# Optimization experiments

Measured on AMD Instinct MI355X. Metric: run time of the kernel, lower is better.

Reference implementation:

```python
import jax, jax.numpy as jnp
import numpy as np

N, C, H, W = 512, 512, 7, 7
K = 64
ALPHA = 100.0
HW = H * W


def _up13(x):
    # bilinear upsample (..., 7, 7) -> (..., 13, 13), align_corners=True
    src = jnp.arange(13, dtype=jnp.float32) * (6.0 / 12.0)
    i0 = jnp.floor(src).astype(jnp.int32)
    i1 = jnp.minimum(i0 + 1, 6)
    w = src - i0.astype(jnp.float32)
    xr = x[..., i0, :] * (1.0 - w)[:, None] + x[..., i1, :] * w[:, None]  # rows
    xc = xr[..., :, i0] * (1.0 - w) + xr[..., :, i1] * w                  # cols
    return xc


def _conv2d(x, w, b, p):
    y = jax.lax.conv_general_dilated(
        x, w, window_strides=(1, 1), padding=[(p, p), (p, p)],
        dimension_numbers=('NCHW', 'OIHW', 'NCHW'))
    return y + b[None, :, None, None]


def setup_inputs() -> dict:
    key = jax.random.key(0)
    ks = jax.random.split(key, 16)
    x = jax.random.normal(ks[0], (N, C, H, W), jnp.float32)
    centroids = jax.random.uniform(ks[1], (K, C), jnp.float32)
    # conv params initialized from centroids as in _init_params (separate params after init)
    conv_w = 2.0 * ALPHA * centroids                    # (K, C) 1x1 conv kernel
    conv_b = -ALPHA * jnp.linalg.norm(centroids, axis=1)
    ln_w = jnp.ones((7, 7), jnp.float32)
    ln_b = jnp.zeros((7, 7), jnp.float32)
    c3_w = 0.02 * jax.random.normal(ks[2], (32, 512, 3, 3), jnp.float32)
    c3_b = jnp.zeros((32,), jnp.float32)
    c5_w = 0.02 * jax.random.normal(ks[3], (32, 512, 5, 5), jnp.float32)
    c5_b = jnp.zeros((32,), jnp.float32)
    c7_w = 0.02 * jax.random.normal(ks[4], (20, 512, 7, 7), jnp.float32)
    c7_b = jnp.zeros((20,), jnp.float32)
    dw_w = 0.1 * jax.random.normal(ks[5], (7, 13), jnp.float32)
    dw_b = jnp.zeros((7,), jnp.float32)
    dh_w = 0.1 * jax.random.normal(ks[6], (7, 13), jnp.float32)
    dh_b = jnp.zeros((7,), jnp.float32)
    acc_w = 0.1 * jax.random.normal(ks[7], (1, 84), jnp.float32)  # 1x1 conv (O, I)
    acc_b = jnp.zeros((1,), jnp.float32)
    return dict(x=x, centroids=centroids, conv_w=conv_w, conv_b=conv_b,
                ln_w=ln_w, ln_b=ln_b, c3_w=c3_w, c3_b=c3_b, c5_w=c5_w, c5_b=c5_b,
                c7_w=c7_w, c7_b=c7_b, dw_w=dw_w, dw_b=dw_b, dh_w=dh_w, dh_b=dh_b,
                acc_w=acc_w, acc_b=acc_b)


def reference(x, centroids, conv_w, conv_b, ln_w, ln_b,
              c3_w, c3_b, c5_w, c5_b, c7_w, c7_b,
              dw_w, dw_b, dh_w, dh_b, acc_w, acc_b):
    # ---- CRN on the raw (un-normalized) input ----
    mu = jnp.mean(x, axis=(-2, -1), keepdims=True)
    var = jnp.mean((x - mu) ** 2, axis=(-2, -1), keepdims=True)
    h = (x - mu) / jnp.sqrt(var + 1e-5) * ln_w + ln_b          # LayerNorm([7,7])
    h = _up13(h)                                               # (N,512,13,13)
    h = jnp.concatenate([_conv2d(h, c3_w, c3_b, 1),
                         _conv2d(h, c5_w, c5_b, 2),
                         _conv2d(h, c7_w, c7_b, 3)], axis=1)   # (N,84,13,13)
    h = jnp.einsum('nchw,ow->ncho', h, dw_w) + dw_b            # width 13->7
    h = h.transpose(0, 1, 3, 2)
    h = jnp.einsum('nchw,ow->ncho', h, dh_w) + dh_b            # height 13->7
    cw = jnp.einsum('nchw,oc->nohw', h, acc_w) + acc_b[None, :, None, None]
    cw = cw.reshape(N, 1, HW)                                  # context weights

    # ---- descriptor-wise L2 normalization over channels ----
    nrm = jnp.sqrt(jnp.sum(x * x, axis=1, keepdims=True))
    xn = x / jnp.maximum(nrm, 1e-12)

    # ---- soft assignment (1x1 conv + softmax over clusters) ----
    logits = (jnp.einsum('nchw,kc->nkhw', xn, conv_w)
              + conv_b[None, :, None, None]).reshape(N, K, HW)
    sa = jax.nn.softmax(logits, axis=1)
    mask = sa * cw                                             # (N,K,HW)

    # ---- fused VLAD aggregation (same math as masked residual sum) ----
    xf = xn.reshape(N, C, HW)
    vlad = jnp.einsum('nkl,ncl->nkc', mask, xf) \
        - centroids[None, :, :] * jnp.sum(mask, axis=-1)[:, :, None]
    vlad = vlad / jnp.maximum(jnp.linalg.norm(vlad, axis=2, keepdims=True), 1e-12)
    vlad = vlad.reshape(N, K * C)
    vlad = vlad / jnp.maximum(jnp.linalg.norm(vlad, axis=1, keepdims=True), 1e-12)
    return vlad
```

## Files before the change

kernel.cpp:

```cpp
#include <hip/hip_runtime.h>
#include <math.h>

#define NI 512
#define CC 512
#define KCL 64
#define HW49 49
#define CQ 25088
#define AP 260
#define GP 68
#define XQP 132

__device__ __forceinline__ float Uval(int i, int u) {
    if (i & 1) return (u == ((i - 1) >> 1) || u == ((i + 1) >> 1)) ? 0.5f : 0.0f;
    return (u == (i >> 1)) ? 1.0f : 0.0f;
}

__global__ __launch_bounds__(256) void kG(
    const float* __restrict__ c3w, const float* __restrict__ c5w, const float* __restrict__ c7w,
    const float* __restrict__ dww, const float* __restrict__ dhw, const float* __restrict__ accw,
    const float* __restrict__ lnw, const float* __restrict__ lnb,
    float* __restrict__ Gmat, float* __restrict__ Gl)
{
    const int c = blockIdx.x;
    const int t = threadIdx.x;
    __shared__ float dh[91], dw[91];
    __shared__ float Fh3[147], Fw3[147], Fh5[245], Fw5[245], Fh7[343], Fw7[343];
    __shared__ float wa3[9], wa5[25], wa7[49];
    __shared__ float Gtmp[2401];
    if (t < 91) dh[t] = dhw[t];
    if (t >= 128 && t < 219) dw[t - 128] = dww[t - 128];
    __syncthreads();
    for (int idx = t; idx < 147; idx += 256) {
        int oh = idx / 21, r = idx % 21, u = r / 3, dy = r % 3;
        float sh = 0.f, sw = 0.f;
        for (int i = 0; i < 13; i++) { int y = i - dy + 1; if (y >= 0 && y < 13) { float uu = Uval(i, u); sh += dh[oh * 13 + y] * uu; sw += dw[oh * 13 + y] * uu; } }
        Fh3[idx] = sh; Fw3[idx] = sw;
    }
    for (int idx = t; idx < 245; idx += 256) {
        int oh = idx / 35, r = idx % 35, u = r / 5, dy = r % 5;
        float sh = 0.f, sw = 0.f;
        for (int i = 0; i < 13; i++) { int y = i - dy + 2; if (y >= 0 && y < 13) { float uu = Uval(i, u); sh += dh[oh * 13 + y] * uu; sw += dw[oh * 13 + y] * uu; } }
        Fh5[idx] = sh; Fw5[idx] = sw;
    }
    for (int idx = t; idx < 343; idx += 256) {
        int oh = idx / 49, r = idx % 49, u = r / 7, dy = r % 7;
        float sh = 0.f, sw = 0.f;
        for (int i = 0; i < 13; i++) { int y = i - dy + 3; if (y >= 0 && y < 13) { float uu = Uval(i, u); sh += dh[oh * 13 + y] * uu; sw += dw[oh * 13 + y] * uu; } }
        Fh7[idx] = sh; Fw7[idx] = sw;
    }
    if (t < 9)               { float s = 0.f; for (int co = 0; co < 32; co++) s += accw[co]      * c3w[(size_t)(co * 512 + c) * 9  + t];        wa3[t] = s; }
    if (t >= 32 && t < 57)   { int q = t - 32; float s = 0.f; for (int co = 0; co < 32; co++) s += accw[32 + co] * c5w[(size_t)(co * 512 + c) * 25 + q]; wa5[q] = s; }
    if (t >= 64 && t < 113)  { int q = t - 64; float s = 0.f; for (int co = 0; co < 20; co++) s += accw[64 + co] * c7w[(size_t)(co * 512 + c) * 49 + q]; wa7[q] = s; }
    __syncthreads();
    for (int o = t; o < 2401; o += 256) {
        int q = o / 49, p = o % 49;
        int u = q / 7, v = q % 7, ow = p / 7, oh = p % 7;
        float acc = 0.f;
        #pragma unroll
        for (int dy = 0; dy < 3; dy++) { float fh = Fh3[(oh * 7 + u) * 3 + dy];
            #pragma unroll
            for (int dx = 0; dx < 3; dx++) acc += wa3[dy * 3 + dx] * fh * Fw3[(ow * 7 + v) * 3 + dx]; }
        #pragma unroll
        for (int dy = 0; dy < 5; dy++) { float fh = Fh5[(oh * 7 + u) * 5 + dy];
            #pragma unroll
            for (int dx = 0; dx < 5; dx++) acc += wa5[dy * 5 + dx] * fh * Fw5[(ow * 7 + v) * 5 + dx]; }
        #pragma unroll
        for (int dy = 0; dy < 7; dy++) { float fh = Fh7[(oh * 7 + u) * 7 + dy];
            #pragma unroll
            for (int dx = 0; dx < 7; dx++) acc += wa7[dy * 7 + dx] * fh * Fw7[(ow * 7 + v) * 7 + dx]; }
        Gtmp[o] = acc;
        Gmat[(size_t)c * 2401 + o] = acc * lnw[q];
    }
    __syncthreads();
    if (t < 49) {
        float s = 0.f;
        for (int q = 0; q < 49; q++) s += Gtmp[q * 49 + t] * lnb[q];
        Gl[c * 49 + t] = s;
    }
}

__global__ void kCb(const float* __restrict__ c3b, const float* __restrict__ c5b, const float* __restrict__ c7b,
                    const float* __restrict__ dww, const float* __restrict__ dwb,
                    const float* __restrict__ dhw, const float* __restrict__ dhb,
                    const float* __restrict__ accw, const float* __restrict__ accb,
                    const float* __restrict__ Gl, float* __restrict__ Cb)
{
    __shared__ float A0s, A1s, Sdw[7], Sdh[7];
    int t = threadIdx.x;
    if (t == 0) {
        float a0 = 0.f, a1 = 0.f;
        for (int co = 0; co < 84; co++) {
            float aw = accw[co]; a0 += aw;
            float b = (co < 32) ? c3b[co] : ((co < 64) ? c5b[co - 32] : c7b[co - 64]);
            a1 += aw * b;
        }
        A0s = a0; A1s = a1;
    }
    if (t < 7)             { float s = 0.f; for (int xx = 0; xx < 13; xx++) s += dww[t * 13 + xx]; Sdw[t] = s; }
    if (t >= 8 && t < 15)  { int oh = t - 8; float s = 0.f; for (int y = 0; y < 13; y++) s += dhw[oh * 13 + y]; Sdh[oh] = s; }
    __syncthreads();
    if (t < 49) {
        int ow = t / 7, oh = t % 7;
        float g = 0.f;
        for (int c = 0; c < 512; c++) g += Gl[c * 49 + t];
        Cb[t] = A1s * Sdw[ow] * Sdh[oh] + A0s * (dwb[ow] * Sdh[oh] + dhb[oh]) + accb[0] + g;
    }
}

__global__ __launch_bounds__(256) void kCw1(const float* __restrict__ x,
    const float* __restrict__ Gmat, float* __restrict__ part)
{
    __shared__ float As[49 * AP];
    __shared__ float Gs[49 * GP];
    const int b = blockIdx.x;
    const int nt = b >> 8, ks = b & 255;
    const int n0 = nt * 256;
    const int t = threadIdx.x;
    const int tn = t >> 3;
    const int tp = t & 7;
    float acc[8][8];
    #pragma unroll
    for (int j = 0; j < 8; j++)
        #pragma unroll
        for (int m = 0; m < 8; m++) acc[j][m] = 0.f;
    for (int kk = 0; kk < 2; kk++) {
        const int c = ks * 2 + kk;
        for (int i = t; i < 12544; i += 256) {
            int nr = i / 49, q = i - nr * 49;
            As[q * AP + nr] = x[(size_t)(n0 + nr) * CQ + (size_t)c * 49 + q];
        }
        for (int i = t; i < 2401; i += 256) {
            int q = i / 49, p = i - q * 49;
            Gs[q * GP + p] = Gmat[(size_t)c * 2401 + i];
        }
        for (int i = t; i < 735; i += 256) {
            int q = i / 15, pc = 49 + (i - q * 15);
            Gs[q * GP + pc] = 0.f;
        }
        __syncthreads();
        {
            float s = 0.f, ss = 0.f;
            for (int q = 0; q < 49; q++) { float v = As[q * AP + t]; s += v; ss += v * v; }
            float mu = s * (1.f / 49.f);
            float var = ss * (1.f / 49.f) - mu * mu;
            float rs = 1.f / sqrtf(var + 1e-5f);
            for (int q = 0; q < 49; q++) As[q * AP + t] = (As[q * AP + t] - mu) * rs;
        }
        __syncthreads();
        for (int q = 0; q < 49; q++) {
            float4 a0 = *(const float4*)&As[q * AP + tn * 8];
            float4 a1 = *(const float4*)&As[q * AP + tn * 8 + 4];
            float4 g0 = *(const float4*)&Gs[q * GP + tp * 8];
            float4 g1 = *(const float4*)&Gs[q * GP + tp * 8 + 4];
            float av[8] = {a0.x, a0.y, a0.z, a0.w, a1.x, a1.y, a1.z, a1.w};
            float gv[8] = {g0.x, g0.y, g0.z, g0.w, g1.x, g1.y, g1.z, g1.w};
            #pragma unroll
            for (int j = 0; j < 8; j++)
                #pragma unroll
                for (int m = 0; m < 8; m++) acc[j][m] += av[j] * gv[m];
        }
        __syncthreads();
    }
    #pragma unroll
    for (int j = 0; j < 8; j++) {
        #pragma unroll
        for (int m = 0; m < 8; m++) {
            int p = tp * 8 + m;
            if (p < 49) As[(tn * 8 + j) * 49 + p] = acc[j][m];
        }
    }
    __syncthreads();
    {
        float* dst = part + (size_t)ks * CQ + (size_t)n0 * 49;
        for (int i = t; i < 12544; i += 256) dst[i] = As[i];
    }
}

__global__ __launch_bounds__(512) void kLog(const float* __restrict__ x,
    const float* __restrict__ convw, const float* __restrict__ convb,
    const float* __restrict__ part, const float* __restrict__ Cbg,
    float* __restrict__ maskr, float* __restrict__ msum)
{
    __shared__ float xq[49 * XQP];
    __shared__ float lg[64 * 52];
    __shared__ float ps[8 * 56];
    __shared__ float rn[49], cwl[49], smax[49], sinv[49];
    __shared__ float cb[64];
    __shared__ float pmx[392], psm[392];
    const int n = blockIdx.x;
    const int t = threadIdx.x;
    const int lane = t & 63;
    const int kw = __builtin_amdgcn_readfirstlane(t >> 6);
    const float* xp = x + (size_t)n * CQ;

    if (t < 392) {
        int p = t >> 3, q = t & 7;
        const float* bp = part + (size_t)(q * 32) * CQ + (size_t)n * 49 + p;
        float s0 = 0.f, s1 = 0.f, s2 = 0.f, s3 = 0.f;
        for (int i = 0; i < 32; i += 4) {
            s0 += bp[(size_t)(i + 0) * CQ];
            s1 += bp[(size_t)(i + 1) * CQ];
            s2 += bp[(size_t)(i + 2) * CQ];
            s3 += bp[(size_t)(i + 3) * CQ];
        }
        psm[t] = (s0 + s1) + (s2 + s3);
    }
    if (t >= 448) cb[t - 448] = convb[t - 448];
    __syncthreads();
    if (t < 49) {
        float s = Cbg[t];
        #pragma unroll
        for (int q = 0; q < 8; q++) s += psm[t * 8 + q];
        cwl[t] = s;
    }

    float a[8] = {0.f, 0.f, 0.f, 0.f, 0.f, 0.f, 0.f, 0.f};
    float rs_part = 0.f;
    for (int qt = 0; qt < 4; qt++) {
        __syncthreads();
        for (int idx = t; idx < 1568; idx += 512) {
            int cg = idx / 49, l = idx - cg * 49;
            const float* src = xp + (size_t)(qt * 128 + cg * 4) * 49 + l;
            float4 v;
            v.x = src[0]; v.y = src[49]; v.z = src[98]; v.w = src[147];
            *(float4*)&xq[l * XQP + cg * 4] = v;
        }
        __syncthreads();
        if (lane < 49) {
            const float* row = &xq[lane * XQP + kw * 16];
            #pragma unroll
            for (int c4 = 0; c4 < 4; c4++) {
                float4 v = *(const float4*)(row + c4 * 4);
                rs_part += v.x * v.x + v.y * v.y + v.z * v.z + v.w * v.w;
            }
        }
        {
            const int lr = (lane < 49) ? lane : 48;
            const float* xrow = &xq[lr * XQP];
            const float* wb = convw + (size_t)(kw * 8) * 512 + qt * 128;
            for (int c4 = 0; c4 < 32; c4++) {
                float4 xv = *(const float4*)(xrow + c4 * 4);
                #pragma unroll
                for (int j = 0; j < 8; j++) {
                    float4 wv = *(const float4*)&wb[j * 512 + c4 * 4];
                    a[j] += wv.x * xv.x + wv.y * xv.y + wv.z * xv.z + wv.w * xv.w;
                }
            }
        }
    }
    if (lane < 49) ps[kw * 56 + lane] = rs_part;
    __syncthreads();
    if (t < 49) {
        float s = 0.f;
        #pragma unroll
        for (int q = 0; q < 8; q++) s += ps[q * 56 + t];
        rn[t] = 1.f / fmaxf(sqrtf(s), 1e-12f);
    }
    __syncthreads();
    if (lane < 49) {
        float r = rn[lane];
        #pragma unroll
        for (int j = 0; j < 8; j++) lg[(kw * 8 + j) * 52 + lane] = a[j] * r + cb[kw * 8 + j];
    }
    __syncthreads();
    if (t < 392) {
        int l = t >> 3, kq = t & 7;
        float m = -3.402823466e38f;
        #pragma unroll
        for (int j = 0; j < 8; j++) m = fmaxf(m, lg[(kq * 8 + j) * 52 + l]);
        pmx[t] = m;
    }
    __syncthreads();
    if (t < 49) {
        float m = pmx[t * 8];
        #pragma unroll
        for (int q = 1; q < 8; q++) m = fmaxf(m, pmx[t * 8 + q]);
        smax[t] = m;
    }
    __syncthreads();
    if (t < 392) {
        int l = t >> 3, kq = t & 7;
        float m = smax[l], s = 0.f;
        #pragma unroll
        for (int j = 0; j < 8; j++) s += __expf(lg[(kq * 8 + j) * 52 + l] - m);
        psm[t] = s;
    }
    __syncthreads();
    if (t < 49) {
        float s = 0.f;
        #pragma unroll
        for (int q = 0; q < 8; q++) s += psm[t * 8 + q];
        sinv[t] = 1.f / s;
    }
    __syncthreads();
    if (t < 392) {
        int l = t >> 3, kq = t & 7;
        float m = smax[l], si = sinv[l] * cwl[l];
        #pragma unroll
        for (int j = 0; j < 8; j++) {
            int idx = (kq * 8 + j) * 52 + l;
            lg[idx] = __expf(lg[idx] - m) * si;
        }
    }
    __syncthreads();
    {
        float msr[8];
        #pragma unroll
        for (int j = 0; j < 8; j++) {
            float s = 0.f;
            for (int l = 0; l < 49; l++) s += lg[(kw * 8 + j) * 52 + l];
            msr[j] = s;
        }
        if (lane == 0) {
            #pragma unroll
            for (int j = 0; j < 8; j++) msum[n * 64 + kw * 8 + j] = msr[j];
        }
    }
    for (int o = t; o < 3136; o += 512) {
        int k = o / 49, l = o - k * 49;
        maskr[(size_t)n * 3136 + o] = lg[k * 52 + l] * rn[l];
    }
}

__global__ __launch_bounds__(512) void kVd(const float* __restrict__ x,
    const float* __restrict__ maskr, const float* __restrict__ msum,
    const float* __restrict__ cent, float* __restrict__ out)
{
    __shared__ float xh[12560];
    __shared__ float lg[64 * 52];
    __shared__ float ssq[64], scl[64];
    const int n = blockIdx.x;
    const int t = threadIdx.x;
    const int lane = t & 63;
    const int kw = __builtin_amdgcn_readfirstlane(t >> 6);
    const float* xp = x + (size_t)n * CQ;
    for (int i = t; i < 3136; i += 512) { int k = i / 49, l = i - k * 49; lg[k * 52 + l] = maskr[(size_t)n * 3136 + i]; }
    for (int i = t; i < 192; i += 512) { lg[(i / 3) * 52 + 49 + (i % 3)] = 0.f; }
    float msr[8];
    #pragma unroll
    for (int j = 0; j < 8; j++) msr[j] = msum[n * 64 + kw * 8 + j];
    const int c0 = lane * 4;
    float accA[8][4], accB[8][4];
    #pragma unroll
    for (int j = 0; j < 8; j++)
        #pragma unroll
        for (int ci = 0; ci < 4; ci++) { accA[j][ci] = 0.f; accB[j][ci] = 0.f; }
    for (int i4 = t; i4 < 3136; i4 += 512)
        *(float4*)&xh[i4 * 4] = *(const float4*)&xp[12544 + i4 * 4];
    if (t < 16) xh[12544 + t] = 0.f;
    __syncthreads();
    for (int lq = 0; lq < 13; lq++) {
        float xr[4][4];
        #pragma unroll
        for (int ci = 0; ci < 4; ci++)
            #pragma unroll
            for (int dl = 0; dl < 4; dl++)
                xr[ci][dl] = xh[(c0 + ci) * 49 + lq * 4 + dl];
        #pragma unroll
        for (int j = 0; j < 8; j++) {
            float4 mv = *(const float4*)&lg[(kw * 8 + j) * 52 + lq * 4];
            #pragma unroll
            for (int ci = 0; ci < 4; ci++)
                accB[j][ci] += mv.x * xr[ci][0] + mv.y * xr[ci][1] + mv.z * xr[ci][2] + mv.w * xr[ci][3];
        }
    }
    __syncthreads();
    for (int i4 = t; i4 < 3136; i4 += 512)
        *(float4*)&xh[i4 * 4] = *(const float4*)&xp[i4 * 4];
    if (t < 16) xh[12544 + t] = 0.f;
    __syncthreads();
    for (int lq = 0; lq < 13; lq++) {
        float xr[4][4];
        #pragma unroll
        for (int ci = 0; ci < 4; ci++)
            #pragma unroll
            for (int dl = 0; dl < 4; dl++)
                xr[ci][dl] = xh[(c0 + ci) * 49 + lq * 4 + dl];
        #pragma unroll
        for (int j = 0; j < 8; j++) {
            float4 mv = *(const float4*)&lg[(kw * 8 + j) * 52 + lq * 4];
            #pragma unroll
            for (int ci = 0; ci < 4; ci++)
                accA[j][ci] += mv.x * xr[ci][0] + mv.y * xr[ci][1] + mv.z * xr[ci][2] + mv.w * xr[ci][3];
        }
    }
    float ssr[8];
    #pragma unroll
    for (int j = 0; j < 8; j++) {
        int k = kw * 8 + j;
        float ms = msr[j];
        float4 ca = *(const float4*)&cent[(size_t)k * 512 + c0];
        float4 cbv = *(const float4*)&cent[(size_t)k * 512 + 256 + c0];
        accA[j][0] -= ca.x * ms; accA[j][1] -= ca.y * ms; accA[j][2] -= ca.z * ms; accA[j][3] -= ca.w * ms;
        accB[j][0] -= cbv.x * ms; accB[j][1] -= cbv.y * ms; accB[j][2] -= cbv.z * ms; accB[j][3] -= cbv.w * ms;
        float s = 0.f;
        #pragma unroll
        for (int ci = 0; ci < 4; ci++) s += accA[j][ci] * accA[j][ci] + accB[j][ci] * accB[j][ci];
        ssr[j] = s;
    }
    #pragma unroll
    for (int j = 0; j < 8; j++)
        for (int off = 32; off >= 1; off >>= 1) ssr[j] += __shfl_xor(ssr[j], off, 64);
    if (lane == 0) {
        #pragma unroll
        for (int j = 0; j < 8; j++) ssq[kw * 8 + j] = ssr[j];
    }
    __syncthreads();
    if (t < 64) {
        float nrm = sqrtf(ssq[t]);
        float inv = 1.f / fmaxf(nrm, 1e-12f);
        float sk = nrm * inv;
        float g = sk * sk;
        #pragma unroll
        for (int off = 32; off >= 1; off >>= 1) g += __shfl_xor(g, off, 64);
        scl[t] = inv * (1.f / fmaxf(sqrtf(g), 1e-12f));
    }
    __syncthreads();
    #pragma unroll
    for (int j = 0; j < 8; j++) {
        int k = kw * 8 + j;
        float s2 = scl[k];
        float4 o1 = make_float4(accA[j][0] * s2, accA[j][1] * s2, accA[j][2] * s2, accA[j][3] * s2);
        float4 o2 = make_float4(accB[j][0] * s2, accB[j][1] * s2, accB[j][2] * s2, accB[j][3] * s2);
        *(float4*)&out[(size_t)n * 32768 + (size_t)k * 512 + c0] = o1;
        *(float4*)&out[(size_t)n * 32768 + (size_t)k * 512 + 256 + c0] = o2;
    }
}

extern "C" void kernel_launch(void* const* d_in, const int* in_sizes, int n_in,
                              void* d_out, int out_size, void* d_ws, size_t ws_size,
                              hipStream_t stream)
{
    const float* x     = (const float*)d_in[0];
    const float* cent  = (const float*)d_in[1];
    const float* convw = (const float*)d_in[2];
    const float* convb = (const float*)d_in[3];
    const float* lnw   = (const float*)d_in[4];
    const float* lnb   = (const float*)d_in[5];
    const float* c3w   = (const float*)d_in[6];
    const float* c3b   = (const float*)d_in[7];
    const float* c5w   = (const float*)d_in[8];
    const float* c5b   = (const float*)d_in[9];
    const float* c7w   = (const float*)d_in[10];
    const float* c7b   = (const float*)d_in[11];
    const float* dww   = (const float*)d_in[12];
    const float* dwb   = (const float*)d_in[13];
    const float* dhw   = (const float*)d_in[14];
    const float* dhb   = (const float*)d_in[15];
    const float* accw  = (const float*)d_in[16];
    const float* accb  = (const float*)d_in[17];
    float* out = (float*)d_out;

    char* ws = (char*)d_ws;
    float* Gmat  = (float*)(ws);
    float* Gl    = (float*)(ws + 4917248);
    float* Cb    = (float*)(ws + 5017600);
    float* part  = (float*)(ws + 5017856);
    float* maskr = (float*)(ws + 30707968);
    float* msumW = (float*)(ws + 37130496);

    kG   <<<512, 256, 0, stream>>>(c3w, c5w, c7w, dww, dhw, accw, lnw, lnb, Gmat, Gl);
    kCb  <<<1,   64,  0, stream>>>(c3b, c5b, c7b, dww, dwb, dhw, dhb, accw, accb, Gl, Cb);
    kCw1 <<<512, 256, 0, stream>>>(x, Gmat, part);
    kLog <<<512, 512, 0, stream>>>(x, convw, convb, part, Cb, maskr, msumW);
    kVd  <<<512, 512, 0, stream>>>(x, maskr, msumW, cent, out);
}
```

Measured before the change: 200.7 us.

## Double-buffer x staging in kLog and stripe channels in kVd to avoid bank conflicts

kLog now prefetches the next 128-channel slice of x into registers and writes it into a second shared-memory buffer while the current slice is being used. This overlaps global loads with the logits dot products and removes one barrier per iteration. The partial-sum reduction is respread across all waves, and the conv bias load moves to the first threads. kVd changes each lane's channels from four contiguous ones to a stride of 64, which avoids LDS bank conflicts on the 49-stride reads, at the cost of scalar rather than float4 centroid loads and output stores.

```diff
diff --git a/kernel.cpp b/kernel.cpp
--- a/kernel.cpp
+++ b/kernel.cpp
@@ -181,7 +181,7 @@
     const float* __restrict__ part, const float* __restrict__ Cbg,
     float* __restrict__ maskr, float* __restrict__ msum)
 {
-    __shared__ float xq[49 * XQP];
+    __shared__ float xq[2][49 * XQP];
     __shared__ float lg[64 * 52];
     __shared__ float ps[8 * 56];
     __shared__ float rn[49], cwl[49], smax[49], sinv[49];
@@ -193,9 +193,22 @@
     const int kw = __builtin_amdgcn_readfirstlane(t >> 6);
     const float* xp = x + (size_t)n * CQ;
 
-    if (t < 392) {
-        int p = t >> 3, q = t & 7;
-        const float* bp = part + (size_t)(q * 32) * CQ + (size_t)n * 49 + p;
+    int scg[4], sl[4];
+    #pragma unroll
+    for (int s = 0; s < 4; s++) {
+        int idx = t + s * 512;
+        scg[s] = idx / 49; sl[s] = idx - scg[s] * 49;
+    }
+    float4 r[4];
+    #pragma unroll
+    for (int s = 0; s < 4; s++) {
+        if (s < 3 || t < 32) {
+            const float* src = xp + (size_t)(scg[s] * 4) * 49 + sl[s];
+            r[s].x = src[0]; r[s].y = src[49]; r[s].z = src[98]; r[s].w = src[147];
+        }
+    }
+    if (lane < 49) {
+        const float* bp = part + (size_t)(kw * 32) * CQ + (size_t)n * 49 + lane;
         float s0 = 0.f, s1 = 0.f, s2 = 0.f, s3 = 0.f;
         for (int i = 0; i < 32; i += 4) {
             s0 += bp[(size_t)(i + 0) * CQ];
@@ -203,9 +216,23 @@
             s2 += bp[(size_t)(i + 2) * CQ];
             s3 += bp[(size_t)(i + 3) * CQ];
         }
-        psm[t] = (s0 + s1) + (s2 + s3);
-    }
-    if (t >= 448) cb[t - 448] = convb[t - 448];
+        psm[lane * 8 + kw] = (s0 + s1) + (s2 + s3);
+    }
+    if (t < 64) cb[t] = convb[t];
+
+    float a[8] = {0.f, 0.f, 0.f, 0.f, 0.f, 0.f, 0.f, 0.f};
+    float rs_part = 0.f;
+
+    #pragma unroll
+    for (int s = 0; s < 4; s++)
+        if (s < 3 || t < 32) *(float4*)&xq[0][sl[s] * XQP + scg[s] * 4] = r[s];
+    #pragma unroll
+    for (int s = 0; s < 4; s++) {
+        if (s < 3 || t < 32) {
+            const float* src = xp + (size_t)(128 + scg[s] * 4) * 49 + sl[s];
+            r[s].x = src[0]; r[s].y = src[49]; r[s].z = src[98]; r[s].w = src[147];
+        }
+    }
     __syncthreads();
     if (t < 49) {
         float s = Cbg[t];
@@ -213,21 +240,10 @@
         for (int q = 0; q < 8; q++) s += psm[t * 8 + q];
         cwl[t] = s;
     }
-
-    float a[8] = {0.f, 0.f, 0.f, 0.f, 0.f, 0.f, 0.f, 0.f};
-    float rs_part = 0.f;
     for (int qt = 0; qt < 4; qt++) {
-        __syncthreads();
-        for (int idx = t; idx < 1568; idx += 512) {
-            int cg = idx / 49, l = idx - cg * 49;
-            const float* src = xp + (size_t)(qt * 128 + cg * 4) * 49 + l;
-            float4 v;
-            v.x = src[0]; v.y = src[49]; v.z = src[98]; v.w = src[147];
-            *(float4*)&xq[l * XQP + cg * 4] = v;
-        }
-        __syncthreads();
+        const float* buf = xq[qt & 1];
         if (lane < 49) {
-            const float* row = &xq[lane * XQP + kw * 16];
+            const float* row = &buf[lane * XQP + kw * 16];
             #pragma unroll
             for (int c4 = 0; c4 < 4; c4++) {
                 float4 v = *(const float4*)(row + c4 * 4);
@@ -236,7 +252,7 @@
         }
         {
             const int lr = (lane < 49) ? lane : 48;
-            const float* xrow = &xq[lr * XQP];
+            const float* xrow = &buf[lr * XQP];
             const float* wb = convw + (size_t)(kw * 8) * 512 + qt * 128;
             for (int c4 = 0; c4 < 32; c4++) {
                 float4 xv = *(const float4*)(xrow + c4 * 4);
@@ -247,6 +263,21 @@
                 }
             }
         }
+        if (qt < 3) {
+            #pragma unroll
+            for (int s = 0; s < 4; s++)
+                if (s < 3 || t < 32) *(float4*)&xq[(qt + 1) & 1][sl[s] * XQP + scg[s] * 4] = r[s];
+            if (qt < 2) {
+                #pragma unroll
+                for (int s = 0; s < 4; s++) {
+                    if (s < 3 || t < 32) {
+                        const float* src = xp + (size_t)((qt + 2) * 128 + scg[s] * 4) * 49 + sl[s];
+                        r[s].x = src[0]; r[s].y = src[49]; r[s].z = src[98]; r[s].w = src[147];
+                    }
+                }
+            }
+            __syncthreads();
+        }
     }
     if (lane < 49) ps[kw * 56 + lane] = rs_part;
     __syncthreads();
@@ -258,9 +289,9 @@
     }
     __syncthreads();
     if (lane < 49) {
-        float r = rn[lane];
-        #pragma unroll
-        for (int j = 0; j < 8; j++) lg[(kw * 8 + j) * 52 + lane] = a[j] * r + cb[kw * 8 + j];
+        float r0 = rn[lane];
+        #pragma unroll
+        for (int j = 0; j < 8; j++) lg[(kw * 8 + j) * 52 + lane] = a[j] * r0 + cb[kw * 8 + j];
     }
     __syncthreads();
     if (t < 392) {
@@ -339,7 +370,6 @@
     float msr[8];
     #pragma unroll
     for (int j = 0; j < 8; j++) msr[j] = msum[n * 64 + kw * 8 + j];
-    const int c0 = lane * 4;
     float accA[8][4], accB[8][4];
     #pragma unroll
     for (int j = 0; j < 8; j++)
@@ -355,7 +385,7 @@
         for (int ci = 0; ci < 4; ci++)
             #pragma unroll
             for (int dl = 0; dl < 4; dl++)
-                xr[ci][dl] = xh[(c0 + ci) * 49 + lq * 4 + dl];
+                xr[ci][dl] = xh[(lane + 64 * ci) * 49 + lq * 4 + dl];
         #pragma unroll
         for (int j = 0; j < 8; j++) {
             float4 mv = *(const float4*)&lg[(kw * 8 + j) * 52 + lq * 4];
@@ -375,7 +405,7 @@
         for (int ci = 0; ci < 4; ci++)
             #pragma unroll
             for (int dl = 0; dl < 4; dl++)
-                xr[ci][dl] = xh[(c0 + ci) * 49 + lq * 4 + dl];
+                xr[ci][dl] = xh[(lane + 64 * ci) * 49 + lq * 4 + dl];
         #pragma unroll
         for (int j = 0; j < 8; j++) {
             float4 mv = *(const float4*)&lg[(kw * 8 + j) * 52 + lq * 4];
@@ -389,13 +419,15 @@
     for (int j = 0; j < 8; j++) {
         int k = kw * 8 + j;
         float ms = msr[j];
-        float4 ca = *(const float4*)&cent[(size_t)k * 512 + c0];
-        float4 cbv = *(const float4*)&cent[(size_t)k * 512 + 256 + c0];
-        accA[j][0] -= ca.x * ms; accA[j][1] -= ca.y * ms; accA[j][2] -= ca.z * ms; accA[j][3] -= ca.w * ms;
-        accB[j][0] -= cbv.x * ms; accB[j][1] -= cbv.y * ms; accB[j][2] -= cbv.z * ms; accB[j][3] -= cbv.w * ms;
         float s = 0.f;
         #pragma unroll
-        for (int ci = 0; ci < 4; ci++) s += accA[j][ci] * accA[j][ci] + accB[j][ci] * accB[j][ci];
+        for (int ci = 0; ci < 4; ci++) {
+            int c = lane + 64 * ci;
+            float va = accA[j][ci] - cent[(size_t)k * 512 + c] * ms;
+            float vb = accB[j][ci] - cent[(size_t)k * 512 + 256 + c] * ms;
+            accA[j][ci] = va; accB[j][ci] = vb;
+            s += va * va + vb * vb;
+        }
         ssr[j] = s;
     }
     #pragma unroll
@@ -420,10 +452,12 @@
     for (int j = 0; j < 8; j++) {
         int k = kw * 8 + j;
         float s2 = scl[k];
-        float4 o1 = make_float4(accA[j][0] * s2, accA[j][1] * s2, accA[j][2] * s2, accA[j][3] * s2);
-        float4 o2 = make_float4(accB[j][0] * s2, accB[j][1] * s2, accB[j][2] * s2, accB[j][3] * s2);
-        *(float4*)&out[(size_t)n * 32768 + (size_t)k * 512 + c0] = o1;
-        *(float4*)&out[(size_t)n * 32768 + (size_t)k * 512 + 256 + c0] = o2;
+        #pragma unroll
+        for (int ci = 0; ci < 4; ci++) {
+            int c = lane + 64 * ci;
+            out[(size_t)n * 32768 + (size_t)k * 512 + c] = accA[j][ci] * s2;
+            out[(size_t)n * 32768 + (size_t)k * 512 + 256 + c] = accB[j][ci] * s2;
+        }
     }
 }
 
```

Measured after the change: 185.9 us. 7.4% less time.
